# Optimization experiments

Measured on AMD Instinct MI355X. Metric: run time of the kernel, lower is better.

The kernel has to match this reference:

```python
import jax, jax.numpy as jnp
import numpy as np

EPS = 1e-05
H, N, F = 1024, 16, 4096  # hidden_dim, state_dim, ffn_dim


def layernorm(x, g, b):
    mu = jnp.mean(x, axis=-1, keepdims=True)
    var = jnp.mean(jnp.square(x - mu), axis=-1, keepdims=True)
    return (x - mu) * jax.lax.rsqrt(var + EPS) * g + b


def setup_inputs() -> dict:
    key = jax.random.key(0)
    ks = jax.random.split(key, 12)
    B, L = 2, 2048
    s = lambda fan_in: 1.0 / np.sqrt(fan_in)
    inp = {
        "x": jax.random.normal(ks[0], (B, L, H), jnp.float32),
        "ln1_g": jnp.ones((H,), jnp.float32),
        "ln1_b": jnp.zeros((H,), jnp.float32),
        "Wd": jax.random.uniform(ks[1], (H, H), jnp.float32, -s(H), s(H)),
        "bd": jnp.zeros((H,), jnp.float32),
        "Wbc": jax.random.uniform(ks[2], (2 * N, H), jnp.float32, -s(H), s(H)),
        "bbc": jnp.zeros((2 * N,), jnp.float32),
        "A_log": jnp.log(jnp.tile(jnp.arange(1, N + 1, dtype=jnp.float32), (H, 1))),
        "D": jnp.ones((H,), jnp.float32),
        "ln2_g": jnp.ones((H,), jnp.float32),
        "ln2_b": jnp.zeros((H,), jnp.float32),
        "W1": jax.random.uniform(ks[3], (F, H), jnp.float32, -s(H), s(H)),
        "b1": jnp.zeros((F,), jnp.float32),
        "W2": jax.random.uniform(ks[4], (H, F), jnp.float32, -s(F), s(F)),
        "b2": jnp.zeros((H,), jnp.float32),
    }
    return inp


def _selective_ssm(xn, delta, Bm, Cm, A, D):
    # xn: (B,L,H)  delta: (B,L,H)  Bm,Cm: (B,L,N)  A: (H,N)  D: (H,)
    Bsz = xn.shape[0]
    # time-major for scan
    xs = (jnp.moveaxis(delta, 1, 0), jnp.moveaxis(Bm, 1, 0),
          jnp.moveaxis(Cm, 1, 0), jnp.moveaxis(xn, 1, 0))

    def step(h, t):
        d_t, b_t, c_t, x_t = t  # (B,H), (B,N), (B,N), (B,H)
        dA = jnp.exp(d_t[:, :, None] * A)                      # (B,H,N)
        dBx = d_t[:, :, None] * b_t[:, None, :] * x_t[:, :, None]
        h = dA * h + dBx                                       # (B,H,N)
        y = jnp.einsum('bhn,bn->bh', h, c_t)                   # (B,H)
        return h, y

    h0 = jnp.zeros((Bsz, H, N), xn.dtype)
    _, ys = jax.lax.scan(step, h0, xs)
    y = jnp.moveaxis(ys, 0, 1)  # (B,L,H)
    return y + D * xn


def reference(x, ln1_g, ln1_b, Wd, bd, Wbc, bbc, A_log, D,
              ln2_g, ln2_b, W1, b1, W2, b2):
    # --- SSMLayer: pre-norm selective SSM + residual ---
    xn = layernorm(x, ln1_g, ln1_b)
    delta = jax.nn.softplus(xn @ Wd.T + bd)      # (B,L,H)
    bc = xn @ Wbc.T + bbc                        # (B,L,2N)
    Bm, Cm = bc[..., :N], bc[..., N:]
    A = -jnp.exp(A_log)                          # (H,N), negative real
    ssm_out = x + _selective_ssm(xn, delta, Bm, Cm, A, D)
    # --- MambaBlock: norm -> FFN -> residual with ssm_out ---
    normed = layernorm(ssm_out, ln2_g, ln2_b)
    hff = jax.nn.gelu(normed @ W1.T + b1, approximate=False)
    ffn_out = hff @ W2.T + b2
    return ffn_out + ssm_out
```

## Files before the change

### kernel.cpp

```cpp
#include <hip/hip_runtime.h>
#include <cstdint>
#include <cstddef>

typedef unsigned short USHORT;
typedef __bf16 bf16x8 __attribute__((ext_vector_type(8)));
typedef float f32x4 __attribute__((ext_vector_type(4)));

__device__ __forceinline__ float b2f(USHORT u) {
    union { unsigned int i; float f; } v; v.i = ((unsigned int)u) << 16; return v.f;
}
__device__ __forceinline__ USHORT f2bf(float f) {
    union { float f; unsigned int i; } v; v.f = f;
    unsigned int u = v.i;
    unsigned int r = (u + 0x7FFFu + ((u >> 16) & 1u)) >> 16;
    return (USHORT)r;
}
__device__ __forceinline__ float fexp2(float x) { return __builtin_amdgcn_exp2f(x); }

__device__ __forceinline__ void gload_lds16(const void* g, void* l) {
    __builtin_amdgcn_global_load_lds(
        (const __attribute__((address_space(1))) void*)(uintptr_t)g,
        (__attribute__((address_space(3))) void*)(uint32_t)(uintptr_t)l,
        16, 0, 0);
}

__global__ __launch_bounds__(256)
void f2b_kernel(const float* __restrict__ src, USHORT* __restrict__ dst, int n)
{
    int i = (blockIdx.x * 256 + threadIdx.x) * 4;
    if (i < n) {
        float4 v = *(const float4*)(src + i);
        ushort4 o;
        o.x = f2bf(v.x); o.y = f2bf(v.y); o.z = f2bf(v.z); o.w = f2bf(v.w);
        *(ushort4*)(dst + i) = o;
    }
}

__global__ __launch_bounds__(256)
void ln_kernel(const float* __restrict__ inp, const float* __restrict__ g,
               const float* __restrict__ bsh, USHORT* __restrict__ out)
{
    const int tid = threadIdx.x;
    const size_t row = blockIdx.x;
    float4 t = ((const float4*)inp)[row * 256 + tid];
    float v[4] = { t.x, t.y, t.z, t.w };
    float s = v[0] + v[1] + v[2] + v[3];
    float sq = v[0]*v[0] + v[1]*v[1] + v[2]*v[2] + v[3]*v[3];
    #pragma unroll
    for (int off = 32; off; off >>= 1) { s += __shfl_down(s, off); sq += __shfl_down(sq, off); }
    __shared__ float red[8];
    const int wv = tid >> 6;
    if ((tid & 63) == 0) { red[wv] = s; red[wv + 4] = sq; }
    __syncthreads();
    const float S  = red[0] + red[1] + red[2] + red[3];
    const float SQ = red[4] + red[5] + red[6] + red[7];
    const float mu = S * (1.0f / 1024.0f);
    const float var = SQ * (1.0f / 1024.0f) - mu * mu;
    const float rs = rsqrtf(var + 1e-5f);
    float4 gv = ((const float4*)g)[tid];
    float4 bv = ((const float4*)bsh)[tid];
    ushort4 o;
    o.x = f2bf((v[0] - mu) * rs * gv.x + bv.x);
    o.y = f2bf((v[1] - mu) * rs * gv.y + bv.y);
    o.z = f2bf((v[2] - mu) * rs * gv.z + bv.z);
    o.w = f2bf((v[3] - mu) * rs * gv.w + bv.w);
    ((ushort4*)out)[row * 256 + tid] = o;
}

template<int EPI>
__global__ __launch_bounds__(256)
void gemm_bt(const USHORT* __restrict__ A, const USHORT* __restrict__ B,
             const float* __restrict__ bias, void* __restrict__ outp,
             void* __restrict__ outp2, int M, int N, int K, int lda, int ldb)
{
    __shared__ __align__(16) unsigned char smem[32768];
    USHORT* As = (USHORT*)smem;
    USHORT* Bs = (USHORT*)(smem + 8192);
    const int tid = threadIdx.x;
    const int lane = tid & 63;
    const int w = tid >> 6;
    const int wr = w >> 1, wc = w & 1;

    const int nx = gridDim.x, ny = gridDim.y;
    const int pid = blockIdx.y * nx + blockIdx.x;
    const int npg = 8 * nx;
    const int gid = pid / npg;
    const int first = gid * 8;
    const int rem = ny - first;
    const int gsz = (rem < 8) ? rem : 8;
    const int py = first + (pid % npg) % gsz;
    const int px = (pid % npg) / gsz;
    const int tm = py * 128;
    const int tn = px * 128;

    USHORT* po = nullptr;
    if constexpr (EPI == 3) {
        const int z = blockIdx.z;
        A += (size_t)z * K;
        B += (size_t)z * K;
        po = ((z < 2) ? (USHORT*)outp : (USHORT*)outp2) + (size_t)(z & 1) * M * N;
    }

    f32x4 acc[4][4];
    #pragma unroll
    for (int i = 0; i < 4; i++)
        #pragma unroll
        for (int j = 0; j < 4; j++) acc[i][j] = (f32x4){0.f, 0.f, 0.f, 0.f};

    const int srow = tid >> 2;
    const int scol = (tid & 3) * 8;
    const USHORT* gA0 = A + (size_t)(tm + srow) * lda + scol;
    const USHORT* gA1 = A + (size_t)(tm + 64 + srow) * lda + scol;
    const USHORT* gB0 = B + (size_t)(tn + srow) * ldb + scol;
    const USHORT* gB1 = B + (size_t)(tn + 64 + srow) * ldb + scol;
    USHORT* lA0 = As + w * 512;
    USHORT* lA1 = As + 2048 + w * 512;
    USHORT* lB0 = Bs + w * 512;
    USHORT* lB1 = Bs + 2048 + w * 512;

    const int fr = lane & 15;
    const int fko = (lane >> 4) * 8;
    const int quad = lane >> 4;

    for (int k0 = 0; k0 < K; k0 += 64) {
        gload_lds16(gA0 + k0, lA0);
        gload_lds16(gA1 + k0, lA1);
        gload_lds16(gB0 + k0, lB0);
        gload_lds16(gB1 + k0, lB1);
        gload_lds16(gA0 + k0 + 32, lA0 + 8192);
        gload_lds16(gA1 + k0 + 32, lA1 + 8192);
        gload_lds16(gB0 + k0 + 32, lB0 + 8192);
        gload_lds16(gB1 + k0 + 32, lB1 + 8192);
        __syncthreads();
        #pragma unroll
        for (int h = 0; h < 2; h++) {
            const USHORT* Ah = As + h * 8192;
            const USHORT* Bh = Bs + h * 8192;
            bf16x8 af[4], bfr[4];
            #pragma unroll
            for (int i = 0; i < 4; i++) {
                af[i]  = *(const bf16x8*)(Ah + (wr * 64 + i * 16 + fr) * 32 + fko);
                bfr[i] = *(const bf16x8*)(Bh + (wc * 64 + i * 16 + fr) * 32 + fko);
            }
            #pragma unroll
            for (int i = 0; i < 4; i++)
                #pragma unroll
                for (int j = 0; j < 4; j++)
                    acc[i][j] = __builtin_amdgcn_mfma_f32_16x16x32_bf16(af[i], bfr[j], acc[i][j], 0, 0, 0);
        }
        __syncthreads();
    }

    float* eW = (float*)(smem + (size_t)w * 4352);
    const int rr = lane >> 5;
    const int cc = lane & 31;
    const int gcolb = tn + wc * 64;
    float2 bvv;
    if constexpr (EPI == 3) { bvv.x = 0.f; bvv.y = 0.f; }
    else bvv = *(const float2*)&bias[gcolb + cc * 2];

    #pragma unroll
    for (int i = 0; i < 4; i++) {
        #pragma unroll
        for (int j = 0; j < 4; j++)
            #pragma unroll
            for (int r = 0; r < 4; r++)
                eW[(quad * 4 + r) * 68 + j * 16 + fr] = acc[i][j][r];
        __syncthreads();
        const int grow0 = tm + wr * 64 + i * 16;
        #pragma unroll
        for (int rp = 0; rp < 8; rp++) {
            const int row = rp * 2 + rr;
            const float2 v = *(const float2*)&eW[row * 68 + cc * 2];
            const size_t gidx = (size_t)(grow0 + row) * N + gcolb + cc * 2;
            if constexpr (EPI == 1) {
                const float z0 = v.x + bvv.x, z1 = v.y + bvv.y;
                const float u0 = z0 * (0.7978845608f + 0.035677408f * z0 * z0);
                const float u1 = z1 * (0.7978845608f + 0.035677408f * z1 * z1);
                const float s0 = __builtin_amdgcn_rcpf(1.f + fexp2(2.885390082f * u0));
                const float s1 = __builtin_amdgcn_rcpf(1.f + fexp2(2.885390082f * u1));
                const float g0 = z0 * (1.f - s0), g1 = z1 * (1.f - s1);
                const uint32_t pk = (uint32_t)f2bf(g0) | ((uint32_t)f2bf(g1) << 16);
                *(uint32_t*)((USHORT*)outp + gidx) = pk;
            } else {
                const uint32_t pk = (uint32_t)f2bf(v.x) | ((uint32_t)f2bf(v.y) << 16);
                *(uint32_t*)(po + gidx) = pk;
            }
        }
        __syncthreads();
    }
}

__global__ __launch_bounds__(256)
void delta_reduce(const USHORT* __restrict__ p, const float* __restrict__ bias,
                  float* __restrict__ out)
{
    const size_t PS = (size_t)4096 * 1024;
    const size_t i = ((size_t)blockIdx.x * 256 + threadIdx.x) * 4;
    ushort4 a = *(const ushort4*)(p + i);
    ushort4 b = *(const ushort4*)(p + PS + i);
    float4 bv = *(const float4*)(bias + (i & 1023));
    float z[4] = { b2f(a.x) + b2f(b.x) + bv.x, b2f(a.y) + b2f(b.y) + bv.y,
                   b2f(a.z) + b2f(b.z) + bv.z, b2f(a.w) + b2f(b.w) + bv.w };
    float4 o;
    o.x = (z[0] > 20.f) ? z[0] : 0.69314718f * __log2f(1.f + fexp2(z[0] * 1.44269504f));
    o.y = (z[1] > 20.f) ? z[1] : 0.69314718f * __log2f(1.f + fexp2(z[1] * 1.44269504f));
    o.z = (z[2] > 20.f) ? z[2] : 0.69314718f * __log2f(1.f + fexp2(z[2] * 1.44269504f));
    o.w = (z[3] > 20.f) ? z[3] : 0.69314718f * __log2f(1.f + fexp2(z[3] * 1.44269504f));
    *(float4*)(out + i) = o;
}

__global__ __launch_bounds__(256)
void ffn2_reduce(const USHORT* __restrict__ p01, const USHORT* __restrict__ p23,
                 const float* __restrict__ bias, const float* __restrict__ extra,
                 float* __restrict__ out)
{
    const size_t PS = (size_t)4096 * 1024;
    const size_t i = ((size_t)blockIdx.x * 256 + threadIdx.x) * 4;
    ushort4 a = *(const ushort4*)(p01 + i);
    ushort4 b = *(const ushort4*)(p01 + PS + i);
    ushort4 c = *(const ushort4*)(p23 + i);
    ushort4 d = *(const ushort4*)(p23 + PS + i);
    float4 bv = *(const float4*)(bias + (i & 1023));
    float4 ev = *(const float4*)(extra + i);
    float4 o;
    o.x = b2f(a.x) + b2f(b.x) + b2f(c.x) + b2f(d.x) + bv.x + ev.x;
    o.y = b2f(a.y) + b2f(b.y) + b2f(c.y) + b2f(d.y) + bv.y + ev.y;
    o.z = b2f(a.z) + b2f(b.z) + b2f(c.z) + b2f(d.z) + bv.z + ev.z;
    o.w = b2f(a.w) + b2f(b.w) + b2f(c.w) + b2f(d.w) + bv.w + ev.w;
    *(float4*)(out + i) = o;
}

__global__ __launch_bounds__(256)
void bc_mfma(const USHORT* __restrict__ xn, const USHORT* __restrict__ WbcB,
             const float* __restrict__ bbc, float* __restrict__ bc)
{
    __shared__ __align__(16) USHORT As[64 * 32];
    __shared__ __align__(16) USHORT Bs[32 * 32];
    const int tid = threadIdx.x;
    const int lane = tid & 63;
    const int w = tid >> 6;
    const int tok0 = blockIdx.x * 64;

    const int srow = tid >> 2;
    const int scol = (tid & 3) * 8;
    const USHORT* gA = xn + (size_t)(tok0 + srow) * 1024 + scol;
    const USHORT* gB = WbcB + (size_t)srow * 1024 + scol;
    USHORT* lA = As + w * 512;
    USHORT* lB = Bs + w * 512;

    const int fr = lane & 15;
    const int fko = (lane >> 4) * 8;
    const int quad = lane >> 4;

    f32x4 acc[2];
    acc[0] = (f32x4){0.f, 0.f, 0.f, 0.f};
    acc[1] = (f32x4){0.f, 0.f, 0.f, 0.f};

    for (int k0 = 0; k0 < 1024; k0 += 32) {
        gload_lds16(gA + k0, lA);
        if (w < 2) gload_lds16(gB + k0, lB);
        __syncthreads();
        bf16x8 af = *(const bf16x8*)(As + (w * 16 + fr) * 32 + fko);
        bf16x8 b0 = *(const bf16x8*)(Bs + (fr) * 32 + fko);
        bf16x8 b1 = *(const bf16x8*)(Bs + (16 + fr) * 32 + fko);
        acc[0] = __builtin_amdgcn_mfma_f32_16x16x32_bf16(af, b0, acc[0], 0, 0, 0);
        acc[1] = __builtin_amdgcn_mfma_f32_16x16x32_bf16(af, b1, acc[1], 0, 0, 0);
        __syncthreads();
    }

    #pragma unroll
    for (int j = 0; j < 2; j++) {
        const int col = j * 16 + fr;
        const float bv = bbc[col];
        #pragma unroll
        for (int r = 0; r < 4; r++) {
            const int row = tok0 + w * 16 + quad * 4 + r;
            bc[(size_t)row * 32 + col] = acc[j][r] + bv;
        }
    }
}

#define SCAN_P 64
#define SCAN_T 32

__global__ __launch_bounds__(256)
void scan_pass1(const USHORT* __restrict__ xn, const float* __restrict__ delta,
                const float* __restrict__ bc, const float* __restrict__ Alog,
                float* __restrict__ sEnd, float* __restrict__ Ptot)
{
    const int tid = threadIdx.x;
    const int h = blockIdx.x * 256 + tid;
    const int b = blockIdx.y;
    const int p = blockIdx.z;
    const size_t tok0 = (size_t)b * 2048 + p * SCAN_T;

    __shared__ __align__(16) float sBC[SCAN_T][32];
    {
        int t = tid >> 3, q = (tid & 7) * 4;
        *(float4*)&sBC[t][q] = *(const float4*)(bc + (tok0 + t) * 32 + q);
    }

    float en[16], s[16], P[16];
    #pragma unroll
    for (int k = 0; k < 4; k++) {
        float4 a = *(const float4*)(Alog + h * 16 + k * 4);
        en[k*4+0] = -__expf(a.x) * 1.44269504f;
        en[k*4+1] = -__expf(a.y) * 1.44269504f;
        en[k*4+2] = -__expf(a.z) * 1.44269504f;
        en[k*4+3] = -__expf(a.w) * 1.44269504f;
    }
    #pragma unroll
    for (int n = 0; n < 16; n++) { s[n] = 0.f; P[n] = 1.f; }
    __syncthreads();

    const float* dp = delta + tok0 * 1024 + h;
    const USHORT* xp = xn + tok0 * 1024 + h;
    float d_c = dp[0];
    USHORT x_c = xp[0];
    for (int t = 0; t < SCAN_T; ++t) {
        const int tn = (t < SCAN_T - 1) ? t + 1 : t;
        float d_n = dp[(size_t)tn * 1024];
        USHORT x_n = xp[(size_t)tn * 1024];
        const float dx = d_c * b2f(x_c);
        #pragma unroll
        for (int k = 0; k < 4; k++) {
            float4 Bv = *(const float4*)&sBC[t][k*4];
            float bb[4] = { Bv.x, Bv.y, Bv.z, Bv.w };
            #pragma unroll
            for (int j = 0; j < 4; j++) {
                const int n = k*4 + j;
                const float dA = fexp2(d_c * en[n]);
                s[n] = fmaf(dA, s[n], dx * bb[j]);
                P[n] *= dA;
            }
        }
        d_c = d_n; x_c = x_n;
    }

    const size_t off = (size_t)p * 32768 + ((size_t)b * 1024 + h) * 16;
    #pragma unroll
    for (int k = 0; k < 4; k++) {
        *(float4*)(sEnd + off + k*4) = (float4){ s[k*4], s[k*4+1], s[k*4+2], s[k*4+3] };
        *(float4*)(Ptot + off + k*4) = (float4){ P[k*4], P[k*4+1], P[k*4+2], P[k*4+3] };
    }
}

__global__ __launch_bounds__(256)
void scan_mid(const float* __restrict__ sEnd, const float* __restrict__ Ptot,
              float* __restrict__ sIn)
{
    const int L = blockIdx.x * 256 + threadIdx.x;
    float s = 0.f;
    #pragma unroll 8
    for (int p = 0; p < SCAN_P; ++p) {
        const size_t off = (size_t)p * 32768 + L;
        sIn[off] = s;
        s = fmaf(Ptot[off], s, sEnd[off]);
    }
}

__global__ __launch_bounds__(256)
void scan_pass2(const float* __restrict__ x, const USHORT* __restrict__ xn,
                const float* __restrict__ delta, const float* __restrict__ bc,
                const float* __restrict__ Alog, const float* __restrict__ Dp,
                const float* __restrict__ sIn, float* __restrict__ ssm)
{
    const int tid = threadIdx.x;
    const int h = blockIdx.x * 256 + tid;
    const int b = blockIdx.y;
    const int p = blockIdx.z;
    const size_t tok0 = (size_t)b * 2048 + p * SCAN_T;

    __shared__ __align__(16) float sBC[SCAN_T][32];
    {
        int t = tid >> 3, q = (tid & 7) * 4;
        *(float4*)&sBC[t][q] = *(const float4*)(bc + (tok0 + t) * 32 + q);
    }

    float en[16], s[16];
    #pragma unroll
    for (int k = 0; k < 4; k++) {
        float4 a = *(const float4*)(Alog + h * 16 + k * 4);
        en[k*4+0] = -__expf(a.x) * 1.44269504f;
        en[k*4+1] = -__expf(a.y) * 1.44269504f;
        en[k*4+2] = -__expf(a.z) * 1.44269504f;
        en[k*4+3] = -__expf(a.w) * 1.44269504f;
    }
    const size_t off = (size_t)p * 32768 + ((size_t)b * 1024 + h) * 16;
    #pragma unroll
    for (int k = 0; k < 4; k++) {
        float4 v = *(const float4*)(sIn + off + k*4);
        s[k*4] = v.x; s[k*4+1] = v.y; s[k*4+2] = v.z; s[k*4+3] = v.w;
    }
    const float Dv = Dp[h];
    __syncthreads();

    const float* dp = delta + tok0 * 1024 + h;
    const USHORT* xp = xn + tok0 * 1024 + h;
    const float* xrp = x + tok0 * 1024 + h;
    float* op = ssm + tok0 * 1024 + h;

    float d_c = dp[0];
    USHORT x_c = xp[0];
    float xr_c = xrp[0];
    for (int t = 0; t < SCAN_T; ++t) {
        const int tn = (t < SCAN_T - 1) ? t + 1 : t;
        float d_n = dp[(size_t)tn * 1024];
        USHORT x_n = xp[(size_t)tn * 1024];
        float xr_n = xrp[(size_t)tn * 1024];
        const float xv = b2f(x_c);
        const float dx = d_c * xv;
        float y = 0.f;
        #pragma unroll
        for (int k = 0; k < 4; k++) {
            float4 Bv = *(const float4*)&sBC[t][k*4];
            float4 Cv = *(const float4*)&sBC[t][16 + k*4];
            float bb[4] = { Bv.x, Bv.y, Bv.z, Bv.w };
            float cc[4] = { Cv.x, Cv.y, Cv.z, Cv.w };
            #pragma unroll
            for (int j = 0; j < 4; j++) {
                const int n = k*4 + j;
                const float dA = fexp2(d_c * en[n]);
                s[n] = fmaf(dA, s[n], dx * bb[j]);
                y = fmaf(cc[j], s[n], y);
            }
        }
        op[(size_t)t * 1024] = xr_c + y + Dv * xv;
        d_c = d_n; x_c = x_n; xr_c = xr_n;
    }
}

extern "C" void kernel_launch(void* const* d_in, const int* in_sizes, int n_in,
                              void* d_out, int out_size, void* d_ws, size_t ws_size,
                              hipStream_t stream)
{
    const float* x    = (const float*)d_in[0];
    const float* ln1g = (const float*)d_in[1];
    const float* ln1b = (const float*)d_in[2];
    const float* Wd   = (const float*)d_in[3];
    const float* bd   = (const float*)d_in[4];
    const float* Wbc  = (const float*)d_in[5];
    const float* bbc  = (const float*)d_in[6];
    const float* Alog = (const float*)d_in[7];
    const float* Dp   = (const float*)d_in[8];
    const float* ln2g = (const float*)d_in[9];
    const float* ln2b = (const float*)d_in[10];
    const float* W1   = (const float*)d_in[11];
    const float* b1   = (const float*)d_in[12];
    const float* W2   = (const float*)d_in[13];
    const float* b2   = (const float*)d_in[14];
    float* out = (float*)d_out;

    char* ws = (char*)d_ws;
    const size_t MB = 1024 * 1024;
    float*  deltaW = (float*)(ws + 0);
    float*  ssmW   = (float*)(ws + 16 * MB);
    USHORT* xnW    = (USHORT*)(ws + 32 * MB);
    USHORT* nrmW   = (USHORT*)(ws + 40 * MB);
    USHORT* hffW   = (USHORT*)(ws + 48 * MB);
    float*  bcW    = (float*)(ws + 80 * MB);
    USHORT* WdB    = (USHORT*)(ws + 81 * MB);
    USHORT* W1B    = (USHORT*)(ws + 83 * MB);
    USHORT* W2B    = (USHORT*)(ws + 91 * MB);
    USHORT* WbcB   = (USHORT*)(ws + 99 * MB);
    USHORT* dpart  = (USHORT*)(ws + 48 * MB);
    float*  sEndW  = (float*)(ws + 48 * MB);
    float*  PtotW  = (float*)(ws + 56 * MB);
    float*  sInW   = (float*)(ws + 64 * MB);
    USHORT* ffn2p01 = (USHORT*)(ws + 0);
    USHORT* ffn2p23 = (USHORT*)(ws + 32 * MB);

    f2b_kernel<<<1024, 256, 0, stream>>>(Wd, WdB, 1024 * 1024);
    f2b_kernel<<<4096, 256, 0, stream>>>(W1, W1B, 4096 * 1024);
    f2b_kernel<<<4096, 256, 0, stream>>>(W2, W2B, 1024 * 4096);
    f2b_kernel<<<32, 256, 0, stream>>>(Wbc, WbcB, 32 * 1024);
    ln_kernel<<<4096, 256, 0, stream>>>(x, ln1g, ln1b, xnW);
    gemm_bt<3><<<dim3(8, 32, 2), 256, 0, stream>>>(xnW, WdB, nullptr, dpart, nullptr, 4096, 1024, 512, 1024, 1024);
    delta_reduce<<<4096, 256, 0, stream>>>(dpart, bd, deltaW);
    bc_mfma<<<64, 256, 0, stream>>>(xnW, WbcB, bbc, bcW);
    scan_pass1<<<dim3(4, 2, SCAN_P), 256, 0, stream>>>(xnW, deltaW, bcW, Alog, sEndW, PtotW);
    scan_mid<<<128, 256, 0, stream>>>(sEndW, PtotW, sInW);
    scan_pass2<<<dim3(4, 2, SCAN_P), 256, 0, stream>>>(x, xnW, deltaW, bcW, Alog, Dp, sInW, ssmW);
    ln_kernel<<<4096, 256, 0, stream>>>(ssmW, ln2g, ln2b, nrmW);
    gemm_bt<1><<<dim3(32, 32), 256, 0, stream>>>(nrmW, W1B, b1, hffW, nullptr, 4096, 4096, 1024, 1024, 1024);
    gemm_bt<3><<<dim3(8, 32, 4), 256, 0, stream>>>(hffW, W2B, nullptr, ffn2p01, ffn2p23, 4096, 1024, 1024, 4096, 4096);
    ffn2_reduce<<<4096, 256, 0, stream>>>(ffn2p01, ffn2p23, b2, ssmW, out);

    (void)in_sizes; (void)n_in; (void)out_size; (void)ws_size;
}
```

Before: 328.0 us.

## Add 256x256 tiled GEMM for FFN and fuse softplus into delta GEMM

Introduces a new 512-thread GEMM kernel with 256x256 tiles, a 4-stage LDS ring buffer fed by direct global-to-LDS loads, XOR-swizzled LDS layout, setprio around MFMA bursts and wider vectorized epilogue stores. It is used for both FFN GEMMs to raise arithmetic intensity and cut LDS bank conflicts. The delta projection now runs without split-K and applies bias plus softplus in its epilogue, removing the partials buffer and the separate reduce kernel. Larger tiles mean fewer workgroups (256 for W1, 256 for split-K W2) and 128KB of LDS per block, so occupancy is one block per CU.

```diff
diff --git a/kernel.cpp b/kernel.cpp
--- a/kernel.cpp
+++ b/kernel.cpp
@@ -93,14 +93,6 @@
     const int tm = py * 128;
     const int tn = px * 128;
 
-    USHORT* po = nullptr;
-    if constexpr (EPI == 3) {
-        const int z = blockIdx.z;
-        A += (size_t)z * K;
-        B += (size_t)z * K;
-        po = ((z < 2) ? (USHORT*)outp : (USHORT*)outp2) + (size_t)(z & 1) * M * N;
-    }
-
     f32x4 acc[4][4];
     #pragma unroll
     for (int i = 0; i < 4; i++)
@@ -155,9 +147,7 @@
     const int rr = lane >> 5;
     const int cc = lane & 31;
     const int gcolb = tn + wc * 64;
-    float2 bvv;
-    if constexpr (EPI == 3) { bvv.x = 0.f; bvv.y = 0.f; }
-    else bvv = *(const float2*)&bias[gcolb + cc * 2];
+    float2 bvv = *(const float2*)&bias[gcolb + cc * 2];
 
     #pragma unroll
     for (int i = 0; i < 4; i++) {
@@ -173,41 +163,166 @@
             const int row = rp * 2 + rr;
             const float2 v = *(const float2*)&eW[row * 68 + cc * 2];
             const size_t gidx = (size_t)(grow0 + row) * N + gcolb + cc * 2;
-            if constexpr (EPI == 1) {
+            if constexpr (EPI == 2) {
                 const float z0 = v.x + bvv.x, z1 = v.y + bvv.y;
+                const float o0 = (z0 > 20.f) ? z0 : 0.69314718f * __log2f(1.f + fexp2(z0 * 1.44269504f));
+                const float o1 = (z1 > 20.f) ? z1 : 0.69314718f * __log2f(1.f + fexp2(z1 * 1.44269504f));
+                *(float2*)((float*)outp + gidx) = make_float2(o0, o1);
+            }
+        }
+        __syncthreads();
+    }
+    (void)outp2; (void)M;
+}
+
+template<int EPI>
+__global__ __launch_bounds__(512)
+void gemm256(const USHORT* __restrict__ A, const USHORT* __restrict__ B,
+             const float* __restrict__ bias, void* __restrict__ outp,
+             void* __restrict__ outp2, int M, int N, int K, int lda, int ldb)
+{
+    __shared__ __align__(16) unsigned char smem[131072];
+    const int tid = threadIdx.x;
+    const int lane = tid & 63;
+    const int w = tid >> 6;
+    const int wr = w >> 2;
+    const int wc = w & 3;
+
+    const int gx = gridDim.x;
+    const int pid = blockIdx.y * gx + blockIdx.x;
+    const int nwg = gx * gridDim.y;
+    const int cpx = nwg >> 3;
+    const int s = (pid & 7) * cpx + (pid >> 3);
+    const int px = s % gx;
+    const int py = s / gx;
+    const int tm = py * 256;
+    const int tn = px * 256;
+
+    USHORT* po = nullptr;
+    if constexpr (EPI == 3) {
+        const int z = blockIdx.z;
+        A += (size_t)z * K;
+        B += (size_t)z * K;
+        po = ((z < 2) ? (USHORT*)outp : (USHORT*)outp2) + (size_t)(z & 1) * ((size_t)M * N);
+    }
+
+    const int sr = tid >> 2;
+    const int su = (tid & 3) ^ ((tid >> 3) & 3);
+    const USHORT* gA0 = A + (size_t)(tm + sr) * lda + su * 8;
+    const USHORT* gA1 = A + (size_t)(tm + 128 + sr) * lda + su * 8;
+    const USHORT* gB0 = B + (size_t)(tn + sr) * ldb + su * 8;
+    const USHORT* gB1 = B + (size_t)(tn + 128 + sr) * ldb + su * 8;
+
+    const int fr = lane & 15;
+    const int quad = lane >> 4;
+    const int uR = quad ^ ((fr >> 1) & 3);
+    const int loff = fr * 32 + uR * 8;
+
+    f32x4 acc[8][4];
+    #pragma unroll
+    for (int i = 0; i < 8; i++)
+        #pragma unroll
+        for (int j = 0; j < 4; j++) acc[i][j] = (f32x4){0.f, 0.f, 0.f, 0.f};
+
+    const int NT = K >> 5;
+
+    auto stage = [&](int t) {
+        unsigned char* sb = smem + (size_t)(t & 3) * 32768;
+        const size_t koff = (size_t)t * 32;
+        gload_lds16(gA0 + koff, sb + w * 1024);
+        gload_lds16(gA1 + koff, sb + 8192 + w * 1024);
+        gload_lds16(gB0 + koff, sb + 16384 + w * 1024);
+        gload_lds16(gB1 + koff, sb + 24576 + w * 1024);
+    };
+
+    stage(0);
+    stage(1);
+
+    for (int t = 0; t < NT; ++t) {
+        if (t + 1 < NT) asm volatile("s_waitcnt vmcnt(4)" ::: "memory");
+        else            asm volatile("s_waitcnt vmcnt(0)" ::: "memory");
+        __builtin_amdgcn_s_barrier();
+        if (t + 2 < NT) stage(t + 2);
+
+        const USHORT* sA = (const USHORT*)(smem + (size_t)(t & 3) * 32768);
+        const USHORT* sB = sA + 8192;
+        bf16x8 a[4], b[4];
+        #pragma unroll
+        for (int j = 0; j < 4; j++)
+            b[j] = *(const bf16x8*)(sB + (wc * 64 + j * 16) * 32 + loff);
+        #pragma unroll
+        for (int i = 0; i < 4; i++)
+            a[i] = *(const bf16x8*)(sA + (wr * 128 + i * 16) * 32 + loff);
+        __builtin_amdgcn_s_setprio(1);
+        #pragma unroll
+        for (int i = 0; i < 4; i++)
+            #pragma unroll
+            for (int j = 0; j < 4; j++)
+                acc[i][j] = __builtin_amdgcn_mfma_f32_16x16x32_bf16(a[i], b[j], acc[i][j], 0, 0, 0);
+        __builtin_amdgcn_s_setprio(0);
+        #pragma unroll
+        for (int i = 0; i < 4; i++)
+            a[i] = *(const bf16x8*)(sA + (wr * 128 + 64 + i * 16) * 32 + loff);
+        __builtin_amdgcn_s_setprio(1);
+        #pragma unroll
+        for (int i = 0; i < 4; i++)
+            #pragma unroll
+            for (int j = 0; j < 4; j++)
+                acc[4 + i][j] = __builtin_amdgcn_mfma_f32_16x16x32_bf16(a[i], b[j], acc[4 + i][j], 0, 0, 0);
+        __builtin_amdgcn_s_setprio(0);
+    }
+
+    float* eW = (float*)(smem + (size_t)w * 4352);
+    const int erow = lane >> 2;
+    const int ecq = lane & 3;
+    const int gcolb = tn + wc * 64 + ecq * 16;
+    float bb[16];
+    if constexpr (EPI == 1) {
+        #pragma unroll
+        for (int q = 0; q < 4; q++) {
+            float4 bv = *(const float4*)&bias[gcolb + q * 4];
+            bb[q*4+0] = bv.x; bb[q*4+1] = bv.y; bb[q*4+2] = bv.z; bb[q*4+3] = bv.w;
+        }
+    }
+    #pragma unroll
+    for (int i = 0; i < 8; i++) {
+        #pragma unroll
+        for (int j = 0; j < 4; j++)
+            #pragma unroll
+            for (int r = 0; r < 4; r++)
+                eW[(quad * 4 + r) * 68 + j * 16 + fr] = acc[i][j][r];
+        float v[16];
+        #pragma unroll
+        for (int q = 0; q < 4; q++) {
+            float4 t4 = *(const float4*)&eW[erow * 68 + ecq * 16 + q * 4];
+            v[q*4+0] = t4.x; v[q*4+1] = t4.y; v[q*4+2] = t4.z; v[q*4+3] = t4.w;
+        }
+        const int grow = tm + wr * 128 + i * 16 + erow;
+        uint32_t pk[8];
+        if constexpr (EPI == 1) {
+            #pragma unroll
+            for (int q = 0; q < 8; q++) {
+                const float z0 = v[2*q]   + bb[2*q];
+                const float z1 = v[2*q+1] + bb[2*q+1];
                 const float u0 = z0 * (0.7978845608f + 0.035677408f * z0 * z0);
                 const float u1 = z1 * (0.7978845608f + 0.035677408f * z1 * z1);
                 const float s0 = __builtin_amdgcn_rcpf(1.f + fexp2(2.885390082f * u0));
                 const float s1 = __builtin_amdgcn_rcpf(1.f + fexp2(2.885390082f * u1));
                 const float g0 = z0 * (1.f - s0), g1 = z1 * (1.f - s1);
-                const uint32_t pk = (uint32_t)f2bf(g0) | ((uint32_t)f2bf(g1) << 16);
-                *(uint32_t*)((USHORT*)outp + gidx) = pk;
-            } else {
-                const uint32_t pk = (uint32_t)f2bf(v.x) | ((uint32_t)f2bf(v.y) << 16);
-                *(uint32_t*)(po + gidx) = pk;
+                pk[q] = (uint32_t)f2bf(g0) | ((uint32_t)f2bf(g1) << 16);
             }
-        }
-        __syncthreads();
-    }
-}
-
-__global__ __launch_bounds__(256)
-void delta_reduce(const USHORT* __restrict__ p, const float* __restrict__ bias,
-                  float* __restrict__ out)
-{
-    const size_t PS = (size_t)4096 * 1024;
-    const size_t i = ((size_t)blockIdx.x * 256 + threadIdx.x) * 4;
-    ushort4 a = *(const ushort4*)(p + i);
-    ushort4 b = *(const ushort4*)(p + PS + i);
-    float4 bv = *(const float4*)(bias + (i & 1023));
-    float z[4] = { b2f(a.x) + b2f(b.x) + bv.x, b2f(a.y) + b2f(b.y) + bv.y,
-                   b2f(a.z) + b2f(b.z) + bv.z, b2f(a.w) + b2f(b.w) + bv.w };
-    float4 o;
-    o.x = (z[0] > 20.f) ? z[0] : 0.69314718f * __log2f(1.f + fexp2(z[0] * 1.44269504f));
-    o.y = (z[1] > 20.f) ? z[1] : 0.69314718f * __log2f(1.f + fexp2(z[1] * 1.44269504f));
-    o.z = (z[2] > 20.f) ? z[2] : 0.69314718f * __log2f(1.f + fexp2(z[2] * 1.44269504f));
-    o.w = (z[3] > 20.f) ? z[3] : 0.69314718f * __log2f(1.f + fexp2(z[3] * 1.44269504f));
-    *(float4*)(out + i) = o;
+            USHORT* op = (USHORT*)outp + (size_t)grow * N + gcolb;
+            *(uint4*)op = make_uint4(pk[0], pk[1], pk[2], pk[3]);
+            *(uint4*)(op + 8) = make_uint4(pk[4], pk[5], pk[6], pk[7]);
+        } else {
+            #pragma unroll
+            for (int q = 0; q < 8; q++)
+                pk[q] = (uint32_t)f2bf(v[2*q]) | ((uint32_t)f2bf(v[2*q+1]) << 16);
+            USHORT* op = po + (size_t)grow * N + gcolb;
+            *(uint4*)op = make_uint4(pk[0], pk[1], pk[2], pk[3]);
+            *(uint4*)(op + 8) = make_uint4(pk[4], pk[5], pk[6], pk[7]);
+        }
+    }
 }
 
 __global__ __launch_bounds__(256)
@@ -464,7 +579,6 @@
     USHORT* W1B    = (USHORT*)(ws + 83 * MB);
     USHORT* W2B    = (USHORT*)(ws + 91 * MB);
     USHORT* WbcB   = (USHORT*)(ws + 99 * MB);
-    USHORT* dpart  = (USHORT*)(ws + 48 * MB);
     float*  sEndW  = (float*)(ws + 48 * MB);
     float*  PtotW  = (float*)(ws + 56 * MB);
     float*  sInW   = (float*)(ws + 64 * MB);
@@ -476,15 +590,14 @@
     f2b_kernel<<<4096, 256, 0, stream>>>(W2, W2B, 1024 * 4096);
     f2b_kernel<<<32, 256, 0, stream>>>(Wbc, WbcB, 32 * 1024);
     ln_kernel<<<4096, 256, 0, stream>>>(x, ln1g, ln1b, xnW);
-    gemm_bt<3><<<dim3(8, 32, 2), 256, 0, stream>>>(xnW, WdB, nullptr, dpart, nullptr, 4096, 1024, 512, 1024, 1024);
-    delta_reduce<<<4096, 256, 0, stream>>>(dpart, bd, deltaW);
+    gemm_bt<2><<<dim3(8, 32), 256, 0, stream>>>(xnW, WdB, bd, deltaW, nullptr, 4096, 1024, 1024, 1024, 1024);
     bc_mfma<<<64, 256, 0, stream>>>(xnW, WbcB, bbc, bcW);
     scan_pass1<<<dim3(4, 2, SCAN_P), 256, 0, stream>>>(xnW, deltaW, bcW, Alog, sEndW, PtotW);
     scan_mid<<<128, 256, 0, stream>>>(sEndW, PtotW, sInW);
     scan_pass2<<<dim3(4, 2, SCAN_P), 256, 0, stream>>>(x, xnW, deltaW, bcW, Alog, Dp, sInW, ssmW);
     ln_kernel<<<4096, 256, 0, stream>>>(ssmW, ln2g, ln2b, nrmW);
-    gemm_bt<1><<<dim3(32, 32), 256, 0, stream>>>(nrmW, W1B, b1, hffW, nullptr, 4096, 4096, 1024, 1024, 1024);
-    gemm_bt<3><<<dim3(8, 32, 4), 256, 0, stream>>>(hffW, W2B, nullptr, ffn2p01, ffn2p23, 4096, 1024, 1024, 4096, 4096);
+    gemm256<1><<<dim3(16, 16), 512, 0, stream>>>(nrmW, W1B, b1, hffW, nullptr, 4096, 4096, 1024, 1024, 1024);
+    gemm256<3><<<dim3(4, 16, 4), 512, 0, stream>>>(hffW, W2B, nullptr, ffn2p01, ffn2p23, 4096, 1024, 1024, 4096, 4096);
     ffn2_reduce<<<4096, 256, 0, stream>>>(ffn2p01, ffn2p23, b2, ssmW, out);
 
     (void)in_sizes; (void)n_in; (void)out_size; (void)ws_size;
```

Result: faster. 306.3 us (-6.6%).
